# Optimization experiments

Measured on AMD Instinct MI355X. Metric: run time of the kernel, lower is better.

Reference implementation:

```python
import jax, jax.numpy as jnp
import numpy as np

N, CIN, COUT, K, H, W = 32, 64, 128, 4, 64, 64


def setup_inputs() -> dict:
    key = jax.random.key(0)
    k1, k2, k3, k4 = jax.random.split(key, 4)
    fan_in = CIN * K * K
    bound = 1.0 / np.sqrt(fan_in)
    x = jax.random.normal(k1, (N, CIN, H, W), dtype=jnp.float32)
    # kaiming_uniform-ish init scale for the conv-transpose weight (Cin, Cout, K, K)
    weight = jax.random.uniform(k2, (CIN, COUT, K, K), dtype=jnp.float32,
                                minval=-bound, maxval=bound)
    conv_bias = jax.random.uniform(k3, (COUT,), dtype=jnp.float32,
                                   minval=-bound, maxval=bound)
    extra_bias = jax.random.normal(k4, (COUT,), dtype=jnp.float32)
    return {"x": x, "weight": weight, "conv_bias": conv_bias, "extra_bias": extra_bias}


def reference(x, weight, conv_bias, extra_bias):
    # ConvTranspose2d(stride=1, pad=0) == conv with spatially flipped kernel and
    # full (K-1) padding. weight is torch IOHW (Cin,Cout,K,K) -> OIHW (Cout,Cin,K,K).
    k = weight.shape[2]
    w_oihw = jnp.flip(weight, (2, 3)).transpose(1, 0, 2, 3)
    y = jax.lax.conv_general_dilated(
        x, w_oihw,
        window_strides=(1, 1),
        padding=[(k - 1, k - 1), (k - 1, k - 1)],
        dimension_numbers=("NCHW", "OIHW", "NCHW"),
    )  # (N, Cout, H+K-1, W+K-1)
    pooled = y.mean(axis=(2, 3)) + conv_bias + extra_bias  # (N, Cout)
    out = 10.0 * jax.nn.logsumexp(pooled, axis=1, keepdims=True)  # (N, 1)
    return out
```

## Files before the change

### kernel.cpp

```cpp
#include <hip/hip_runtime.h>

#define Nn     32
#define CIN    64
#define COUT   128
#define HWVOL  4096
#define PLANES (Nn * CIN)
#define WBLKS  ((CIN * COUT) / 256)
#define OHW_INV (1.0f / 4489.0f)

__global__ __launch_bounds__(256) void stage1_kernel(
    const float* __restrict__ x,
    const float* __restrict__ w,
    float* __restrict__ Sx,
    float* __restrict__ Sw)
{
    const int b = blockIdx.x;
    const int t = threadIdx.x;

    if (b < PLANES) {
        const float4* xp = (const float4*)(x + (size_t)b * HWVOL);
        float acc = 0.0f;
#pragma unroll
        for (int j = 0; j < 4; ++j) {
            float4 v = xp[t + 256 * j];
            acc += (v.x + v.y) + (v.z + v.w);
        }
#pragma unroll
        for (int off = 32; off > 0; off >>= 1)
            acc += __shfl_down(acc, off, 64);
        __shared__ float part[4];
        if ((t & 63) == 0) part[t >> 6] = acc;
        __syncthreads();
        if (t == 0) Sx[b] = (part[0] + part[1]) + (part[2] + part[3]);
    } else {
        const int o = (b - PLANES) * 256 + t;
        const float4* wp = (const float4*)(w + (size_t)o * 16);
        float4 a = wp[0], c = wp[1], d = wp[2], e = wp[3];
        Sw[o] = (((a.x + a.y) + (a.z + a.w)) + ((c.x + c.y) + (c.z + c.w))) +
                (((d.x + d.y) + (d.z + d.w)) + ((e.x + e.y) + (e.z + e.w)));
    }
}

__global__ __launch_bounds__(128) void final_kernel(
    const float* __restrict__ Sx,
    const float* __restrict__ Sw,
    const float* __restrict__ conv_bias,
    const float* __restrict__ extra_bias,
    float* __restrict__ out)
{
    const int n  = blockIdx.x;
    const int co = threadIdx.x;
    __shared__ float sxs[CIN];
    if (co < CIN) sxs[co] = Sx[n * CIN + co];
    __syncthreads();

    float acc = 0.0f;
#pragma unroll
    for (int ci = 0; ci < CIN; ++ci)
        acc = fmaf(sxs[ci], Sw[ci * COUT + co], acc);

    const float pooled = acc * OHW_INV + conv_bias[co] + extra_bias[co];

    float m = pooled;
#pragma unroll
    for (int off = 32; off > 0; off >>= 1)
        m = fmaxf(m, __shfl_xor(m, off, 64));
    __shared__ float wm[2];
    if ((co & 63) == 0) wm[co >> 6] = m;
    __syncthreads();
    m = fmaxf(wm[0], wm[1]);

    float e = __expf(pooled - m);
#pragma unroll
    for (int off = 32; off > 0; off >>= 1)
        e += __shfl_xor(e, off, 64);
    __shared__ float wl[2];
    if ((co & 63) == 0) wl[co >> 6] = e;
    __syncthreads();
    if (co == 0) out[n] = 10.0f * (m + logf(wl[0] + wl[1]));
}

extern "C" void kernel_launch(void* const* d_in, const int* in_sizes, int n_in,
                              void* d_out, int out_size, void* d_ws, size_t ws_size,
                              hipStream_t stream) {
    const float* x          = (const float*)d_in[0];
    const float* weight     = (const float*)d_in[1];
    const float* conv_bias  = (const float*)d_in[2];
    const float* extra_bias = (const float*)d_in[3];
    float* out = (float*)d_out;

    float* Sx = (float*)d_ws;
    float* Sw = Sx + PLANES;

    stage1_kernel<<<PLANES + WBLKS, 256, 0, stream>>>(x, weight, Sx, Sw);
    final_kernel<<<Nn, 128, 0, stream>>>(Sx, Sw, conv_bias, extra_bias, out);
}
```

Before: 78.99 us.

## Fuse plane reduction and logsumexp into one cooperative kernel with grid sync

Replaces the two-kernel sequence with a single cooperative launch of 1024 blocks. Each block sums two input planes, and the first blocks also reduce the weight taps. A grid-wide barrier follows, after which 32 blocks compute the channel contraction and logsumexp. The intent is to remove the second kernel launch and the gap between the two stages, at the cost of a grid barrier and halving the number of blocks that stream the input. If the cooperative launch fails, it falls back to the original two kernels.

```diff
diff --git a/kernel.cpp b/kernel.cpp
--- a/kernel.cpp
+++ b/kernel.cpp
@@ -1,4 +1,7 @@
 #include <hip/hip_runtime.h>
+#include <hip/hip_cooperative_groups.h>
+
+namespace cg = cooperative_groups;
 
 #define Nn     32
 #define CIN    64
@@ -6,7 +9,89 @@
 #define HWVOL  4096
 #define PLANES (Nn * CIN)
 #define WBLKS  ((CIN * COUT) / 256)
+#define GRID   1024
 #define OHW_INV (1.0f / 4489.0f)
+#define NEGBIG (-3.0e38f)
+
+__global__ __launch_bounds__(256, 4) void fused_kernel(
+    const float* __restrict__ x,
+    const float* __restrict__ w,
+    const float* __restrict__ conv_bias,
+    const float* __restrict__ extra_bias,
+    float* __restrict__ Sx,
+    float* __restrict__ Sw,
+    float* __restrict__ out)
+{
+    const int b = blockIdx.x;
+    const int t = threadIdx.x;
+
+    {
+        const float4* p0 = (const float4*)(x + (size_t)b * HWVOL);
+        const float4* p1 = (const float4*)(x + (size_t)(b + GRID) * HWVOL);
+        float a0 = 0.0f, a1 = 0.0f;
+#pragma unroll
+        for (int j = 0; j < 4; ++j) {
+            float4 u = p0[t + 256 * j];
+            float4 v = p1[t + 256 * j];
+            a0 += (u.x + u.y) + (u.z + u.w);
+            a1 += (v.x + v.y) + (v.z + v.w);
+        }
+#pragma unroll
+        for (int off = 32; off > 0; off >>= 1) {
+            a0 += __shfl_down(a0, off, 64);
+            a1 += __shfl_down(a1, off, 64);
+        }
+        __shared__ float part0[4], part1[4];
+        if ((t & 63) == 0) { part0[t >> 6] = a0; part1[t >> 6] = a1; }
+        __syncthreads();
+        if (t == 0)  Sx[b]        = (part0[0] + part0[1]) + (part0[2] + part0[3]);
+        if (t == 64) Sx[b + GRID] = (part1[0] + part1[1]) + (part1[2] + part1[3]);
+
+        if (b < WBLKS) {
+            const int o = b * 256 + t;
+            const float4* wp = (const float4*)(w + (size_t)o * 16);
+            float4 a = wp[0], c = wp[1], d = wp[2], e = wp[3];
+            Sw[o] = (((a.x + a.y) + (a.z + a.w)) + ((c.x + c.y) + (c.z + c.w))) +
+                    (((d.x + d.y) + (d.z + d.w)) + ((e.x + e.y) + (e.z + e.w)));
+        }
+    }
+
+    cg::this_grid().sync();
+
+    if (b >= Nn) return;
+    const int n = b;
+
+    __shared__ float sxs[CIN];
+    if (t < CIN) sxs[t] = Sx[n * CIN + t];
+    __syncthreads();
+
+    float pooled = NEGBIG;
+    if (t < COUT) {
+        float acc = 0.0f;
+#pragma unroll 8
+        for (int ci = 0; ci < CIN; ++ci)
+            acc = fmaf(sxs[ci], Sw[ci * COUT + t], acc);
+        pooled = acc * OHW_INV + conv_bias[t] + extra_bias[t];
+    }
+
+    float m = pooled;
+#pragma unroll
+    for (int off = 32; off > 0; off >>= 1)
+        m = fmaxf(m, __shfl_xor(m, off, 64));
+    __shared__ float wm[4];
+    if ((t & 63) == 0) wm[t >> 6] = m;
+    __syncthreads();
+    m = fmaxf(fmaxf(wm[0], wm[1]), fmaxf(wm[2], wm[3]));
+
+    float e = __expf(pooled - m);
+#pragma unroll
+    for (int off = 32; off > 0; off >>= 1)
+        e += __shfl_xor(e, off, 64);
+    __shared__ float wl[4];
+    if ((t & 63) == 0) wl[t >> 6] = e;
+    __syncthreads();
+    if (t == 0) out[n] = 10.0f * (m + logf((wl[0] + wl[1]) + (wl[2] + wl[3])));
+}
 
 __global__ __launch_bounds__(256) void stage1_kernel(
     const float* __restrict__ x,
@@ -92,6 +177,11 @@
     float* Sx = (float*)d_ws;
     float* Sw = Sx + PLANES;
 
-    stage1_kernel<<<PLANES + WBLKS, 256, 0, stream>>>(x, weight, Sx, Sw);
-    final_kernel<<<Nn, 128, 0, stream>>>(Sx, Sw, conv_bias, extra_bias, out);
+    void* args[] = {&x, &weight, &conv_bias, &extra_bias, &Sx, &Sw, &out};
+    hipError_t err = hipLaunchCooperativeKernel(
+        fused_kernel, dim3(GRID), dim3(256), args, 0u, stream);
+    if (err != hipSuccess) {
+        stage1_kernel<<<PLANES + WBLKS, 256, 0, stream>>>(x, weight, Sx, Sw);
+        final_kernel<<<Nn, 128, 0, stream>>>(Sx, Sw, conv_bias, extra_bias, out);
+    }
 }
```

Result: slower. 170.5 us (+115.9%).
